# Performance work log

Hardware: AMD Instinct MI355X
Metric: run time of the kernel (lower is better)

Reference implementation:

```python
import jax, jax.numpy as jnp
import numpy as np

D_MODEL = 1024
NHEAD = 16
D_K = D_MODEL // NHEAD
BATCH = 8
SEQ = 1024
SPARSITY = 0.9


def setup_inputs() -> dict:
    key = jax.random.key(0)
    ks = jax.random.split(key, 13)
    q = jax.random.normal(ks[0], (BATCH, SEQ, D_MODEL), dtype=jnp.float32)
    k = jax.random.normal(ks[1], (BATCH, SEQ, D_MODEL), dtype=jnp.float32)
    v = jax.random.normal(ks[2], (BATCH, SEQ, D_MODEL), dtype=jnp.float32)
    mask = jax.random.uniform(ks[3], (BATCH, NHEAD, SEQ, SEQ)) > SPARSITY
    s = 1.0 / np.sqrt(D_MODEL)  # nn.Linear-style init scale
    def lin(kw, kb):
        W = jax.random.uniform(kw, (D_MODEL, D_MODEL), minval=-s, maxval=s, dtype=jnp.float32)
        b = jax.random.uniform(kb, (D_MODEL,), minval=-s, maxval=s, dtype=jnp.float32)
        return W, b
    Wq, bq = lin(ks[4], ks[5])
    Wk, bk = lin(ks[6], ks[7])
    Wv, bv = lin(ks[8], ks[9])
    Wo, bo = lin(ks[10], ks[11])
    return {"query": q, "key": k, "value": v, "mask": mask,
            "Wq": Wq, "bq": bq, "Wk": Wk, "bk": bk,
            "Wv": Wv, "bv": bv, "Wo": Wo, "bo": bo}


def reference(query, key, value, mask, Wq, bq, Wk, bk, Wv, bv, Wo, bo):
    B, S, _ = query.shape
    # projections (torch Linear: x @ W.T + b), split into heads -> [B, H, S, d_k]
    def proj(x, W, b):
        return (x @ W.T + b).reshape(B, S, NHEAD, D_K).transpose(0, 2, 1, 3)
    Q = proj(query, Wq, bq)
    K = proj(key, Wk, bk)
    V = proj(value, Wv, bv)
    scale = 1.0 / jnp.sqrt(jnp.float32(D_K))
    scores = jnp.einsum('bhqd,bhkd->bhqk', Q, K) * scale  # [B,H,S,S]
    scores = jnp.where(mask, scores, -jnp.inf)
    attn = jax.nn.softmax(scores, axis=-1)
    out = jnp.einsum('bhqk,bhkd->bhqd', attn, V)           # [B,H,S,d_k]
    out = out.transpose(0, 2, 1, 3).reshape(B, S, D_MODEL)
    return out @ Wo.T + bo
```

## Files before the change

### kernel.cpp

```cpp
#include <hip/hip_runtime.h>

typedef __bf16 bf16;
typedef bf16 bf16x4 __attribute__((ext_vector_type(4)));
typedef bf16 bf16x8 __attribute__((ext_vector_type(8)));
typedef float f32x4 __attribute__((ext_vector_type(4)));

#define D_MODEL 1024
#define NHEAD   16
#define D_K     64
#define BATCH   8
#define SEQL    1024
#define MROWS   (BATCH*SEQL)

struct Cvt7 {
    const float* s[7];
    bf16*        d[7];
    int          n[7];
};

__global__ __launch_bounds__(256) void cvt7_kernel(Cvt7 a) {
    const int y = blockIdx.y;
    const float* __restrict__ src = a.s[y];
    bf16* __restrict__ dst = a.d[y];
    const int n4 = a.n[y] >> 2;
    const int stride = gridDim.x * blockDim.x;
    for (int i = blockIdx.x * blockDim.x + threadIdx.x; i < n4; i += stride) {
        float4 v = ((const float4*)src)[i];
        bf16x4 o = { (bf16)v.x, (bf16)v.y, (bf16)v.z, (bf16)v.w };
        ((bf16x4*)dst)[i] = o;
    }
}

#define BM 128
#define BN 128
#define BK 32

__device__ __forceinline__ void gemm_core(const bf16* __restrict__ A, const bf16* __restrict__ B,
                                          int bm, int bn, int K,
                                          bf16* lA, bf16* lB, f32x4 (&acc)[4][4]) {
    const int t = threadIdx.x;
    const int lane = t & 63, w = t >> 6;
    const int wr = w >> 1, wc = w & 1;
    const int r = lane & 15, kb = lane >> 4;

    for (int k0 = 0; k0 < K; k0 += BK) {
        __syncthreads();
        #pragma unroll
        for (int i = 0; i < 2; ++i) {
            const int off = i * 4096 + w * 1024 + lane * 16;
            const int row = off >> 6;
            const int cb  = off & 63;
            const bf16* srcA = A + (size_t)(bm + row) * K + k0 + (cb >> 1);
            const bf16* srcB = B + (size_t)(bn + row) * K + k0 + (cb >> 1);
            __builtin_amdgcn_global_load_lds(
                (const __attribute__((address_space(1))) unsigned int*)srcA,
                (__attribute__((address_space(3))) unsigned int*)((char*)lA + i * 4096 + w * 1024),
                16, 0, 0);
            __builtin_amdgcn_global_load_lds(
                (const __attribute__((address_space(1))) unsigned int*)srcB,
                (__attribute__((address_space(3))) unsigned int*)((char*)lB + i * 4096 + w * 1024),
                16, 0, 0);
        }
        __syncthreads();

        bf16x8 af[4], bfr[4];
        #pragma unroll
        for (int m = 0; m < 4; ++m)
            af[m] = *(const bf16x8*)(lA + (wr * 64 + m * 16 + r) * BK + kb * 8);
        #pragma unroll
        for (int n = 0; n < 4; ++n)
            bfr[n] = *(const bf16x8*)(lB + (wc * 64 + n * 16 + r) * BK + kb * 8);
        #pragma unroll
        for (int m = 0; m < 4; ++m)
            #pragma unroll
            for (int n = 0; n < 4; ++n)
                acc[m][n] = __builtin_amdgcn_mfma_f32_16x16x32_bf16(af[m], bfr[n], acc[m][n], 0, 0, 0);
    }
}

__global__ __launch_bounds__(256) void proj3_kernel(
        const bf16* __restrict__ xq, const bf16* __restrict__ xk, const bf16* __restrict__ xv,
        const bf16* __restrict__ Wqb, const bf16* __restrict__ Wkb, const bf16* __restrict__ Wvb,
        const float* __restrict__ bq, const float* __restrict__ bk, const float* __restrict__ bv,
        bf16* __restrict__ Qp, bf16* __restrict__ Kp, bf16* __restrict__ Vt) {
    __shared__ bf16 lA[BM * BK], lB[BN * BK];
    const int z = blockIdx.z;
    const bf16* A    = (z == 0) ? xq  : (z == 1) ? xk  : xv;
    const bf16* Bm   = (z == 0) ? Wqb : (z == 1) ? Wkb : Wvb;
    const float* bias = (z == 0) ? bq : (z == 1) ? bk  : bv;
    const int bm = blockIdx.x * BM, bn = blockIdx.y * BN;

    f32x4 acc[4][4] = {};
    gemm_core(A, Bm, bm, bn, D_MODEL, lA, lB, acc);

    const int lane = threadIdx.x & 63, w = threadIdx.x >> 6;
    const int wr = w >> 1, wc = w & 1, r = lane & 15, g = lane >> 4;
    #pragma unroll
    for (int n = 0; n < 4; ++n) {
        const int col = bn + wc * 64 + n * 16 + r;
        const float bvl = bias[col];
        const int h = col >> 6, d = col & 63;
        #pragma unroll
        for (int m = 0; m < 4; ++m) {
            #pragma unroll
            for (int j = 0; j < 4; ++j) {
                const int row = bm + wr * 64 + m * 16 + g * 4 + j;
                const float v = acc[m][n][j] + bvl;
                const int b = row >> 10, s = row & (SEQL - 1);
                const int bh = b * NHEAD + h;
                if (z == 0) {
                    Qp[((size_t)bh * SEQL + s) * D_K + d] = (bf16)v;
                } else if (z == 1) {
                    Kp[((size_t)bh * SEQL + s) * D_K + d] = (bf16)v;
                } else {
                    Vt[((size_t)bh * D_K + d) * SEQL + s] = (bf16)v;
                }
            }
        }
    }
}

__global__ __launch_bounds__(256) void outproj_kernel(
        const bf16* __restrict__ AO, const bf16* __restrict__ Wob,
        const float* __restrict__ bo, float* __restrict__ out) {
    __shared__ bf16 lA[BM * BK], lB[BN * BK];
    const int bm = blockIdx.x * BM, bn = blockIdx.y * BN;
    f32x4 acc[4][4] = {};
    gemm_core(AO, Wob, bm, bn, D_MODEL, lA, lB, acc);

    const int lane = threadIdx.x & 63, w = threadIdx.x >> 6;
    const int wr = w >> 1, wc = w & 1, r = lane & 15, g = lane >> 4;
    #pragma unroll
    for (int n = 0; n < 4; ++n) {
        const int col = bn + wc * 64 + n * 16 + r;
        const float bvl = bo[col];
        #pragma unroll
        for (int m = 0; m < 4; ++m)
            #pragma unroll
            for (int j = 0; j < 4; ++j) {
                const int row = bm + wr * 64 + m * 16 + g * 4 + j;
                out[(size_t)row * D_MODEL + col] = acc[m][n][j] + bvl;
            }
    }
}

__global__ __launch_bounds__(256, 3) void attn_kernel(
        const bf16* __restrict__ Qp, const bf16* __restrict__ Kp, const bf16* __restrict__ Vt,
        const unsigned int* __restrict__ mask, bf16* __restrict__ AO) {
    __shared__ char kbuf[8192];
    __shared__ char vbuf[8192];
    __shared__ char mbuf[16384];
    __shared__ bf16 plds[4][16 * 64];
    const int bh = blockIdx.y, b = bh >> 4, h = bh & 15;
    const int t = threadIdx.x, lane = t & 63, w = t >> 6;
    const int q0 = blockIdx.x * 64;
    const int r = lane & 15, g = lane >> 4;

    const char* __restrict__ Kb = (const char*)(Kp + (size_t)bh * SEQL * D_K);
    const char* __restrict__ Vb = (const char*)(Vt + (size_t)bh * D_K * SEQL);
    const char* __restrict__ Mb = (const char*)(mask + ((size_t)bh * SEQL + q0) * SEQL);

    const bf16* __restrict__ Qh = Qp + ((size_t)bh * SEQL + q0 + w * 16) * D_K;
    bf16x8 qf[2];
    #pragma unroll
    for (int kk = 0; kk < 2; ++kk)
        qf[kk] = *(const bf16x8*)(Qh + r * D_K + kk * 32 + g * 8);

    f32x4 o[4] = {};
    float psum = 0.f;
    char* P = (char*)plds[w];
    const int swz = (r & 7) << 4;

    for (int s0 = 0; s0 < SEQL; s0 += 64) {
        __syncthreads();
        #pragma unroll
        for (int i = 0; i < 2; ++i) {
            const int slot = i * 256 + t;
            const int row = slot >> 3, ch = slot & 7;
            const char* srcK = Kb + (size_t)(s0 + row) * 128 + ((ch * 16) ^ ((row & 7) << 4));
            const char* srcV = Vb + (size_t)row * (SEQL * 2) + s0 * 2 + ((ch * 16) ^ ((row & 7) << 4));
            __builtin_amdgcn_global_load_lds(
                (const __attribute__((address_space(1))) unsigned int*)srcK,
                (__attribute__((address_space(3))) unsigned int*)(kbuf + i * 4096 + w * 1024),
                16, 0, 0);
            __builtin_amdgcn_global_load_lds(
                (const __attribute__((address_space(1))) unsigned int*)srcV,
                (__attribute__((address_space(3))) unsigned int*)(vbuf + i * 4096 + w * 1024),
                16, 0, 0);
        }
        #pragma unroll
        for (int i = 0; i < 4; ++i) {
            const int slot = i * 256 + t;
            const int row = slot >> 4, ch = slot & 15;
            const char* srcM = Mb + (size_t)row * (SEQL * 4) + s0 * 4 + ((ch * 16) ^ ((row & 7) << 4));
            __builtin_amdgcn_global_load_lds(
                (const __attribute__((address_space(1))) unsigned int*)srcM,
                (__attribute__((address_space(3))) unsigned int*)(mbuf + i * 4096 + w * 1024),
                16, 0, 0);
        }
        __syncthreads();

        f32x4 sf[4] = {};
        __builtin_amdgcn_s_setprio(1);
        #pragma unroll
        for (int n = 0; n < 4; ++n) {
            #pragma unroll
            for (int kk = 0; kk < 2; ++kk) {
                const int krow = n * 16 + r;
                bf16x8 kf = *(const bf16x8*)(kbuf + krow * 128 + ((kk * 64 + g * 16) ^ swz));
                sf[n] = __builtin_amdgcn_mfma_f32_16x16x32_bf16(kf, qf[kk], sf[n], 0, 0, 0);
            }
        }
        __builtin_amdgcn_s_setprio(0);
        const int mrow = w * 16 + r;
        #pragma unroll
        for (int n = 0; n < 4; ++n) {
            const uint4 mv = *(const uint4*)(mbuf + mrow * 256 + ((n * 64 + g * 16) ^ swz));
            const float p0 = mv.x ? __expf(sf[n][0] * 0.125f) : 0.f;
            const float p1 = mv.y ? __expf(sf[n][1] * 0.125f) : 0.f;
            const float p2 = mv.z ? __expf(sf[n][2] * 0.125f) : 0.f;
            const float p3 = mv.w ? __expf(sf[n][3] * 0.125f) : 0.f;
            psum += (p0 + p1) + (p2 + p3);
            bf16x4 pb = { (bf16)p0, (bf16)p1, (bf16)p2, (bf16)p3 };
            *(bf16x4*)(P + ((r * 128 + n * 32 + g * 8) ^ swz)) = pb;
        }
        bf16x8 pf0 = *(const bf16x8*)(P + ((r * 128 + 0 * 64 + g * 16) ^ swz));
        bf16x8 pf1 = *(const bf16x8*)(P + ((r * 128 + 1 * 64 + g * 16) ^ swz));
        __builtin_amdgcn_s_setprio(1);
        #pragma unroll
        for (int n = 0; n < 4; ++n) {
            const int vrow = n * 16 + r;
            bf16x8 vf0 = *(const bf16x8*)(vbuf + vrow * 128 + ((0 * 64 + g * 16) ^ swz));
            bf16x8 vf1 = *(const bf16x8*)(vbuf + vrow * 128 + ((1 * 64 + g * 16) ^ swz));
            o[n] = __builtin_amdgcn_mfma_f32_16x16x32_bf16(vf0, pf0, o[n], 0, 0, 0);
            o[n] = __builtin_amdgcn_mfma_f32_16x16x32_bf16(vf1, pf1, o[n], 0, 0, 0);
        }
        __builtin_amdgcn_s_setprio(0);
    }

    psum += __shfl_xor(psum, 16);
    psum += __shfl_xor(psum, 32);
    const float inv = 1.0f / psum;

    const size_t rowbase = ((size_t)(b * SEQL + q0 + w * 16 + r)) * D_MODEL + h * D_K;
    #pragma unroll
    for (int n = 0; n < 4; ++n) {
        bf16x4 ob = { (bf16)(o[n][0] * inv), (bf16)(o[n][1] * inv),
                      (bf16)(o[n][2] * inv), (bf16)(o[n][3] * inv) };
        *(bf16x4*)(AO + rowbase + n * 16 + g * 4) = ob;
    }
}

extern "C" void kernel_launch(void* const* d_in, const int* in_sizes, int n_in,
                              void* d_out, int out_size, void* d_ws, size_t ws_size,
                              hipStream_t stream) {
    const float* q    = (const float*)d_in[0];
    const float* k    = (const float*)d_in[1];
    const float* v    = (const float*)d_in[2];
    const unsigned int* mask = (const unsigned int*)d_in[3];
    const float* Wq = (const float*)d_in[4];
    const float* bq = (const float*)d_in[5];
    const float* Wk = (const float*)d_in[6];
    const float* bk = (const float*)d_in[7];
    const float* Wv = (const float*)d_in[8];
    const float* bv = (const float*)d_in[9];
    const float* Wo = (const float*)d_in[10];
    const float* bo = (const float*)d_in[11];

    char* ws = (char*)d_ws;
    const size_t MB = 1u << 20;
    bf16* qb  = (bf16*)(ws + 0 * MB);
    bf16* kb  = (bf16*)(ws + 16 * MB);
    bf16* vb  = (bf16*)(ws + 32 * MB);
    bf16* Wqb = (bf16*)(ws + 48 * MB);
    bf16* Wkb = (bf16*)(ws + 50 * MB);
    bf16* Wvb = (bf16*)(ws + 52 * MB);
    bf16* Wob = (bf16*)(ws + 54 * MB);
    bf16* Qp  = (bf16*)(ws + 56 * MB);
    bf16* Kp  = (bf16*)(ws + 72 * MB);
    bf16* Vt  = (bf16*)(ws + 88 * MB);
    bf16* AO  = (bf16*)(ws + 104 * MB);

    Cvt7 c;
    c.s[0] = q;  c.d[0] = qb;  c.n[0] = MROWS * D_MODEL;
    c.s[1] = k;  c.d[1] = kb;  c.n[1] = MROWS * D_MODEL;
    c.s[2] = v;  c.d[2] = vb;  c.n[2] = MROWS * D_MODEL;
    c.s[3] = Wq; c.d[3] = Wqb; c.n[3] = D_MODEL * D_MODEL;
    c.s[4] = Wk; c.d[4] = Wkb; c.n[4] = D_MODEL * D_MODEL;
    c.s[5] = Wv; c.d[5] = Wvb; c.n[5] = D_MODEL * D_MODEL;
    c.s[6] = Wo; c.d[6] = Wob; c.n[6] = D_MODEL * D_MODEL;
    cvt7_kernel<<<dim3(1024, 7), 256, 0, stream>>>(c);

    proj3_kernel<<<dim3(MROWS / BM, D_MODEL / BN, 3), 256, 0, stream>>>(
        qb, kb, vb, Wqb, Wkb, Wvb, bq, bk, bv, Qp, Kp, Vt);

    attn_kernel<<<dim3(SEQL / 64, BATCH * NHEAD), 256, 0, stream>>>(Qp, Kp, Vt, mask, AO);

    outproj_kernel<<<dim3(MROWS / BM, D_MODEL / BN), 256, 0, stream>>>(AO, Wob, bo, (float*)d_out);
}
```

Baseline: 292.8 us.

## Double-buffer K/V/mask tiles in attention and remap blocks per XCD

```diff
diff --git a/kernel.cpp b/kernel.cpp
--- a/kernel.cpp
+++ b/kernel.cpp
@@ -144,21 +144,57 @@
     }
 }
 
-__global__ __launch_bounds__(256, 3) void attn_kernel(
+#define NT (SEQL / 64)
+
+__device__ __forceinline__ void stage_tile(const char* __restrict__ Kb, const char* __restrict__ Vb,
+                                           const char* __restrict__ Mb, int s0,
+                                           char* dst, int t, int w) {
+    #pragma unroll
+    for (int i = 0; i < 2; ++i) {
+        const int slot = i * 256 + t;
+        const int row = slot >> 3, ch = slot & 7;
+        const char* srcK = Kb + (size_t)(s0 + row) * 128 + ((ch * 16) ^ ((row & 7) << 4));
+        const char* srcV = Vb + (size_t)row * (SEQL * 2) + s0 * 2 + ((ch * 16) ^ ((row & 7) << 4));
+        __builtin_amdgcn_global_load_lds(
+            (const __attribute__((address_space(1))) unsigned int*)srcK,
+            (__attribute__((address_space(3))) unsigned int*)(dst + i * 4096 + w * 1024),
+            16, 0, 0);
+        __builtin_amdgcn_global_load_lds(
+            (const __attribute__((address_space(1))) unsigned int*)srcV,
+            (__attribute__((address_space(3))) unsigned int*)(dst + 8192 + i * 4096 + w * 1024),
+            16, 0, 0);
+    }
+    #pragma unroll
+    for (int i = 0; i < 4; ++i) {
+        const int slot = i * 256 + t;
+        const int row = slot >> 4, ch = slot & 15;
+        const char* srcM = Mb + (size_t)row * (SEQL * 4) + s0 * 4 + ((ch * 16) ^ ((row & 7) << 4));
+        __builtin_amdgcn_global_load_lds(
+            (const __attribute__((address_space(1))) unsigned int*)srcM,
+            (__attribute__((address_space(3))) unsigned int*)(dst + 16384 + i * 4096 + w * 1024),
+            16, 0, 0);
+    }
+}
+
+__global__ __launch_bounds__(256, 2) void attn_kernel(
         const bf16* __restrict__ Qp, const bf16* __restrict__ Kp, const bf16* __restrict__ Vt,
         const unsigned int* __restrict__ mask, bf16* __restrict__ AO) {
-    __shared__ char kbuf[8192];
-    __shared__ char vbuf[8192];
-    __shared__ char mbuf[16384];
+    __shared__ char sbuf[2][32768];
     __shared__ bf16 plds[4][16 * 64];
-    const int bh = blockIdx.y, b = bh >> 4, h = bh & 15;
+    const int lin = blockIdx.x + blockIdx.y * gridDim.x;
+    const int xcd = lin & 7, pos = lin >> 3;
+    const int bh  = xcd * 16 + (pos & 15);
+    const int qt  = pos >> 4;
+    const int b = bh >> 4, h = bh & 15;
     const int t = threadIdx.x, lane = t & 63, w = t >> 6;
-    const int q0 = blockIdx.x * 64;
+    const int q0 = qt * 64;
     const int r = lane & 15, g = lane >> 4;
 
     const char* __restrict__ Kb = (const char*)(Kp + (size_t)bh * SEQL * D_K);
     const char* __restrict__ Vb = (const char*)(Vt + (size_t)bh * D_K * SEQL);
     const char* __restrict__ Mb = (const char*)(mask + ((size_t)bh * SEQL + q0) * SEQL);
+
+    stage_tile(Kb, Vb, Mb, 0, sbuf[0], t, w);
 
     const bf16* __restrict__ Qh = Qp + ((size_t)bh * SEQL + q0 + w * 16) * D_K;
     bf16x8 qf[2];
@@ -171,34 +207,15 @@
     char* P = (char*)plds[w];
     const int swz = (r & 7) << 4;
 
-    for (int s0 = 0; s0 < SEQL; s0 += 64) {
-        __syncthreads();
-        #pragma unroll
-        for (int i = 0; i < 2; ++i) {
-            const int slot = i * 256 + t;
-            const int row = slot >> 3, ch = slot & 7;
-            const char* srcK = Kb + (size_t)(s0 + row) * 128 + ((ch * 16) ^ ((row & 7) << 4));
-            const char* srcV = Vb + (size_t)row * (SEQL * 2) + s0 * 2 + ((ch * 16) ^ ((row & 7) << 4));
-            __builtin_amdgcn_global_load_lds(
-                (const __attribute__((address_space(1))) unsigned int*)srcK,
-                (__attribute__((address_space(3))) unsigned int*)(kbuf + i * 4096 + w * 1024),
-                16, 0, 0);
-            __builtin_amdgcn_global_load_lds(
-                (const __attribute__((address_space(1))) unsigned int*)srcV,
-                (__attribute__((address_space(3))) unsigned int*)(vbuf + i * 4096 + w * 1024),
-                16, 0, 0);
-        }
-        #pragma unroll
-        for (int i = 0; i < 4; ++i) {
-            const int slot = i * 256 + t;
-            const int row = slot >> 4, ch = slot & 15;
-            const char* srcM = Mb + (size_t)row * (SEQL * 4) + s0 * 4 + ((ch * 16) ^ ((row & 7) << 4));
-            __builtin_amdgcn_global_load_lds(
-                (const __attribute__((address_space(1))) unsigned int*)srcM,
-                (__attribute__((address_space(3))) unsigned int*)(mbuf + i * 4096 + w * 1024),
-                16, 0, 0);
-        }
-        __syncthreads();
+    for (int tt = 0; tt < NT; ++tt) {
+        char* buf = sbuf[tt & 1];
+        if (tt + 1 < NT) {
+            stage_tile(Kb, Vb, Mb, (tt + 1) * 64, sbuf[(tt + 1) & 1], t, w);
+            asm volatile("s_waitcnt vmcnt(8)" ::: "memory");
+        } else {
+            asm volatile("s_waitcnt vmcnt(0)" ::: "memory");
+        }
+        __builtin_amdgcn_s_barrier();
 
         f32x4 sf[4] = {};
         __builtin_amdgcn_s_setprio(1);
@@ -207,7 +224,7 @@
             #pragma unroll
             for (int kk = 0; kk < 2; ++kk) {
                 const int krow = n * 16 + r;
-                bf16x8 kf = *(const bf16x8*)(kbuf + krow * 128 + ((kk * 64 + g * 16) ^ swz));
+                bf16x8 kf = *(const bf16x8*)(buf + krow * 128 + ((kk * 64 + g * 16) ^ swz));
                 sf[n] = __builtin_amdgcn_mfma_f32_16x16x32_bf16(kf, qf[kk], sf[n], 0, 0, 0);
             }
         }
@@ -215,7 +232,7 @@
         const int mrow = w * 16 + r;
         #pragma unroll
         for (int n = 0; n < 4; ++n) {
-            const uint4 mv = *(const uint4*)(mbuf + mrow * 256 + ((n * 64 + g * 16) ^ swz));
+            const uint4 mv = *(const uint4*)(buf + 16384 + mrow * 256 + ((n * 64 + g * 16) ^ swz));
             const float p0 = mv.x ? __expf(sf[n][0] * 0.125f) : 0.f;
             const float p1 = mv.y ? __expf(sf[n][1] * 0.125f) : 0.f;
             const float p2 = mv.z ? __expf(sf[n][2] * 0.125f) : 0.f;
@@ -230,12 +247,13 @@
         #pragma unroll
         for (int n = 0; n < 4; ++n) {
             const int vrow = n * 16 + r;
-            bf16x8 vf0 = *(const bf16x8*)(vbuf + vrow * 128 + ((0 * 64 + g * 16) ^ swz));
-            bf16x8 vf1 = *(const bf16x8*)(vbuf + vrow * 128 + ((1 * 64 + g * 16) ^ swz));
+            bf16x8 vf0 = *(const bf16x8*)(buf + 8192 + vrow * 128 + ((0 * 64 + g * 16) ^ swz));
+            bf16x8 vf1 = *(const bf16x8*)(buf + 8192 + vrow * 128 + ((1 * 64 + g * 16) ^ swz));
             o[n] = __builtin_amdgcn_mfma_f32_16x16x32_bf16(vf0, pf0, o[n], 0, 0, 0);
             o[n] = __builtin_amdgcn_mfma_f32_16x16x32_bf16(vf1, pf1, o[n], 0, 0, 0);
         }
         __builtin_amdgcn_s_setprio(0);
+        __builtin_amdgcn_s_barrier();
     }
 
     psum += __shfl_xor(psum, 16);
```

After: 310.5 us. 1.06x slower.
